# Kernel tuning notes

Measured on AMD Instinct MI355X. Metric: run time of the kernel, lower is better.

Reference implementation:

```python
import jax, jax.numpy as jnp
from jax import lax
import numpy as np

S, B, I, H, O = 65536, 1, 2, 128, 1


def setup_inputs() -> dict:
    key = jax.random.key(0)
    k1, k2, k3, k4 = jax.random.split(key, 4)
    # xavier_normal-style scales
    s_ih = (2.0 / (4 * H + I)) ** 0.5
    s_hh = (2.0 / (4 * H + H)) ** 0.5
    s_out = (2.0 / (H + O)) ** 0.5
    return {
        "x": jax.random.normal(k1, (S, B, I), jnp.float32),
        "h0": jnp.zeros((1, B, H), jnp.float32),
        "c0": jnp.zeros((1, B, H), jnp.float32),
        "W_ih": jax.random.normal(k2, (4 * H, I), jnp.float32) * s_ih,
        "W_hh": jax.random.normal(k3, (4 * H, H), jnp.float32) * s_hh,
        "b_ih": jnp.zeros((4 * H,), jnp.float32),
        "b_hh": jnp.zeros((4 * H,), jnp.float32),
        "W_out": jax.random.normal(k4, (O, H), jnp.float32) * s_out,
        "b_out": jnp.zeros((O,), jnp.float32),
    }


def reference(x, h0, c0, W_ih, W_hh, b_ih, b_hh, W_out, b_out):
    # Precompute input-to-gate projections for all timesteps: (S, B, 4H)
    xg = jnp.einsum("sbi,gi->sbg", x, W_ih) + b_ih + b_hh

    def step(carry, xg_t):
        h, c = carry  # (B, H) each
        gates = xg_t + h @ W_hh.T  # (B, 4H); PyTorch order i,f,g,o
        i, f, g, o = jnp.split(gates, 4, axis=-1)
        i = jax.nn.sigmoid(i)
        f = jax.nn.sigmoid(f)
        g = jnp.tanh(g)
        o = jax.nn.sigmoid(o)
        c = f * c + i * g
        h = o * jnp.tanh(c)
        return (h, c), h

    (_, _), hs = lax.scan(step, (h0[0], c0[0]), xg)  # hs: (S, B, H)
    out = jnp.tanh(hs.transpose(1, 0, 2))  # (B, S, H), matches permute(1,0,2)
    out = out @ W_out.T + b_out  # (B, S, O)
    return out.reshape(out.shape[0] * out.shape[1], -1)  # (B*S, O)
```

## Files before the change

kernel.cpp:

```cpp
#include <hip/hip_runtime.h>

#define S_LEN 65536
#define HDIM 128

typedef _Float16 half2_t __attribute__((ext_vector_type(2)));
typedef _Float16 half8_t __attribute__((ext_vector_type(8)));
typedef float f32x4 __attribute__((ext_vector_type(4)));

__device__ __forceinline__ float sigm(float x) {
    return 1.0f / (1.0f + __expf(-x));
}
__device__ __forceinline__ float tanh_fast(float x) {
    return 2.0f / (1.0f + __expf(-2.0f * x)) - 1.0f;
}
__device__ __forceinline__ float dot2(half2_t a, half2_t b, float c) {
#if __has_builtin(__builtin_amdgcn_fdot2)
    return __builtin_amdgcn_fdot2(a, b, c, false);
#else
    return fmaf((float)a.x, (float)b.x, fmaf((float)a.y, (float)b.y, c));
#endif
}

#define WG_BARRIER() do {                                         \
    asm volatile("s_waitcnt lgkmcnt(0)" ::: "memory");            \
    __builtin_amdgcn_s_barrier();                                 \
    asm volatile("" ::: "memory");                                \
} while (0)

__global__ __launch_bounds__(320)
__attribute__((amdgpu_waves_per_eu(2)))
void lstm_seq_dot2(const float* __restrict__ x,
                   const float* __restrict__ h0,
                   const float* __restrict__ c0,
                   const float* __restrict__ W_ih,
                   const float* __restrict__ W_hh,
                   const float* __restrict__ b_ih,
                   const float* __restrict__ b_hh,
                   _Float16* __restrict__ h_hist)
{
    __shared__ __align__(16) _Float16 h_buf[2][HDIM];
    __shared__ __align__(16) float xb[1024];

    const int tid  = threadIdx.x;
    const int lane = tid & 63;
    const int w    = tid >> 6;

    if (w < 4) {
        const int j    = lane & 31;
        const int half = lane >> 5;
        const int hidx = w * 32 + j;
        const int k0   = half * 64;

#define LW2(g, k2) \
        half2_t w_##g##_##k2; { \
            const float* s_ = W_hh + (size_t)(hidx + 128 * (g)) * HDIM \
                                   + k0 + 2 * (k2); \
            w_##g##_##k2 = (half2_t){ (_Float16)s_[0], (_Float16)s_[1] }; \
            asm volatile("" : "+v"(w_##g##_##k2)); }
#define LWG(g) \
        LW2(g,0)  LW2(g,1)  LW2(g,2)  LW2(g,3)  LW2(g,4)  LW2(g,5)  LW2(g,6)  LW2(g,7)  \
        LW2(g,8)  LW2(g,9)  LW2(g,10) LW2(g,11) LW2(g,12) LW2(g,13) LW2(g,14) LW2(g,15) \
        LW2(g,16) LW2(g,17) LW2(g,18) LW2(g,19) LW2(g,20) LW2(g,21) LW2(g,22) LW2(g,23) \
        LW2(g,24) LW2(g,25) LW2(g,26) LW2(g,27) LW2(g,28) LW2(g,29) LW2(g,30) LW2(g,31)
        LWG(0) LWG(1) LWG(2) LWG(3)
#undef LWG
#undef LW2

        const int r0 = hidx, r1 = hidx + 128, r2 = hidx + 256, r3 = hidx + 384;
        const float wi00 = W_ih[2 * r0], wi01 = W_ih[2 * r0 + 1];
        const float wi10 = W_ih[2 * r1], wi11 = W_ih[2 * r1 + 1];
        const float wi20 = W_ih[2 * r2], wi21 = W_ih[2 * r2 + 1];
        const float wi30 = W_ih[2 * r3], wi31 = W_ih[2 * r3 + 1];
        const float bs0 = b_ih[r0] + b_hh[r0];
        const float bs1 = b_ih[r1] + b_hh[r1];
        const float bs2 = b_ih[r2] + b_hh[r2];
        const float bs3 = b_ih[r3] + b_hh[r3];
        float c = c0[hidx];

        if (tid < HDIM) h_buf[0][tid] = (_Float16)h0[tid];
        __syncthreads();

        const half8_t* hb0 = ((const half8_t*)h_buf[0]) + 8 * half;
        const half8_t* hb1 = ((const half8_t*)h_buf[1]) + 8 * half;

#define PR(hv, p) ((half2_t)__builtin_shufflevector((hv), (hv), 2*(p), 2*(p)+1))

#define GDOT(g, dst) { \
        float A_=0.f, B_=0.f, C_=0.f, D_=0.f; \
        A_=dot2(w_##g##_0 , PR(hv0,0), A_); B_=dot2(w_##g##_1 , PR(hv0,1), B_); \
        C_=dot2(w_##g##_2 , PR(hv0,2), C_); D_=dot2(w_##g##_3 , PR(hv0,3), D_); \
        A_=dot2(w_##g##_4 , PR(hv1,0), A_); B_=dot2(w_##g##_5 , PR(hv1,1), B_); \
        C_=dot2(w_##g##_6 , PR(hv1,2), C_); D_=dot2(w_##g##_7 , PR(hv1,3), D_); \
        A_=dot2(w_##g##_8 , PR(hv2,0), A_); B_=dot2(w_##g##_9 , PR(hv2,1), B_); \
        C_=dot2(w_##g##_10, PR(hv2,2), C_); D_=dot2(w_##g##_11, PR(hv2,3), D_); \
        A_=dot2(w_##g##_12, PR(hv3,0), A_); B_=dot2(w_##g##_13, PR(hv3,1), B_); \
        C_=dot2(w_##g##_14, PR(hv3,2), C_); D_=dot2(w_##g##_15, PR(hv3,3), D_); \
        A_=dot2(w_##g##_16, PR(hv4,0), A_); B_=dot2(w_##g##_17, PR(hv4,1), B_); \
        C_=dot2(w_##g##_18, PR(hv4,2), C_); D_=dot2(w_##g##_19, PR(hv4,3), D_); \
        A_=dot2(w_##g##_20, PR(hv5,0), A_); B_=dot2(w_##g##_21, PR(hv5,1), B_); \
        C_=dot2(w_##g##_22, PR(hv5,2), C_); D_=dot2(w_##g##_23, PR(hv5,3), D_); \
        A_=dot2(w_##g##_24, PR(hv6,0), A_); B_=dot2(w_##g##_25, PR(hv6,1), B_); \
        C_=dot2(w_##g##_26, PR(hv6,2), C_); D_=dot2(w_##g##_27, PR(hv6,3), D_); \
        A_=dot2(w_##g##_28, PR(hv7,0), A_); B_=dot2(w_##g##_29, PR(hv7,1), B_); \
        C_=dot2(w_##g##_30, PR(hv7,2), C_); D_=dot2(w_##g##_31, PR(hv7,3), D_); \
        dst = (A_ + B_) + (C_ + D_); }

#define STEP(T, RB, WB) { \
        const half8_t* hb_ = (RB); \
        half8_t hv0 = hb_[0], hv1 = hb_[1], hv2 = hb_[2], hv3 = hb_[3]; \
        half8_t hv4 = hb_[4], hv5 = hb_[5], hv6 = hb_[6], hv7 = hb_[7]; \
        const float2 xv = *(const float2*)(xb + 2 * ((T) & 511)); \
        float s0, s1, s2, s3; \
        GDOT(1, s1)  s1 += __shfl_xor(s1, 32, 64); \
        GDOT(0, s0)  s0 += __shfl_xor(s0, 32, 64); \
        GDOT(2, s2)  s2 += __shfl_xor(s2, 32, 64); \
        GDOT(3, s3)  s3 += __shfl_xor(s3, 32, 64); \
        const float gf = sigm(fmaf(wi10, xv.x, fmaf(wi11, xv.y, bs1)) + s1); \
        const float gi = sigm(fmaf(wi00, xv.x, fmaf(wi01, xv.y, bs0)) + s0); \
        const float gg = tanh_fast(fmaf(wi20, xv.x, fmaf(wi21, xv.y, bs2)) + s2); \
        const float go = sigm(fmaf(wi30, xv.x, fmaf(wi31, xv.y, bs3)) + s3); \
        c = fmaf(gf, c, gi * gg); \
        const float hval = go * tanh_fast(c); \
        const _Float16 hf_ = (_Float16)hval; \
        if (lane < 32) (WB)[hidx] = hf_; \
        WG_BARRIER(); }

        #pragma unroll 1
        for (int t = 0; t < S_LEN; t += 2) {
            STEP(t,     hb0, h_buf[1])
            STEP(t + 1, hb1, h_buf[0])
        }
#undef STEP
#undef GDOT
#undef PR
    } else {
        {
            const float4* src = (const float4*)x + lane;
            float4 a0 = src[0], a1 = src[64], a2 = src[128], a3 = src[192];
            float4* dst = (float4*)xb + lane;
            dst[0] = a0; dst[64] = a1; dst[128] = a2; dst[192] = a3;
        }
        __syncthreads();

        float4 xs0 = {0.f, 0.f, 0.f, 0.f}, xs1 = xs0;

        #pragma unroll 1
        for (int t = 0; t < S_LEN; ++t) {
            const int r   = t & 255;
            const int blk = t >> 8;
            if (r == 0 && blk >= 1 && blk < 255) {
                const float4* src = (const float4*)x
                                  + (size_t)(blk + 1) * 128 + lane;
                xs0 = src[0]; xs1 = src[64];
            }
            if (r == 128 && blk >= 1 && blk < 255) {
                float4* dst = (float4*)xb + (((blk + 1) & 1) * 128) + lane;
                dst[0] = xs0; dst[64] = xs1;
            }
            if (t > 0) {
                const uint32_t hv_ =
                    *(const uint32_t*)((const char*)(h_buf[t & 1]) + 4 * lane);
                ((uint32_t*)h_hist)[(size_t)(t - 1) * 64 + lane] = hv_;
            }
            WG_BARRIER();
        }
        const uint32_t hv_ =
            *(const uint32_t*)((const char*)(h_buf[0]) + 4 * lane);
        ((uint32_t*)h_hist)[(size_t)(S_LEN - 1) * 64 + lane] = hv_;
    }
}

__global__ __launch_bounds__(256)
void out_proj(const _Float16* __restrict__ h_hist,
              const float* __restrict__ W_out,
              const float* __restrict__ b_out,
              float* __restrict__ out)
{
    const int lane  = threadIdx.x & 63;
    const int gwave = (blockIdx.x * 256 + threadIdx.x) >> 6;
    const int nwave = (gridDim.x * 256) >> 6;

    const float wo0 = W_out[2 * lane + 0];
    const float wo1 = W_out[2 * lane + 1];
    const float bout = b_out[0];

    for (int t = gwave; t < S_LEN; t += nwave) {
        half2_t hv = ((const half2_t*)(h_hist + t * HDIM))[lane];
        float p = tanh_fast((float)hv.x) * wo0 + tanh_fast((float)hv.y) * wo1;
        #pragma unroll
        for (int off = 32; off > 0; off >>= 1)
            p += __shfl_xor(p, off, 64);
        if (lane == 0) out[t] = p + bout;
    }
}

#define H_HI_OFF 144
__global__ __launch_bounds__(1024)
__attribute__((amdgpu_waves_per_eu(4, 4)))
void lstm_seq_full(const float* __restrict__ x,
                   const float* __restrict__ h0,
                   const float* __restrict__ c0,
                   const float* __restrict__ W_ih,
                   const float* __restrict__ W_hh,
                   const float* __restrict__ b_ih,
                   const float* __restrict__ b_hh,
                   const float* __restrict__ W_out,
                   const float* __restrict__ b_out,
                   float* __restrict__ out)
{
    __shared__ __align__(16) unsigned char h_raw[2 * H_HI_OFF];
    __shared__ float gates_part[2 * 512];
    __shared__ float red_sh[2];

    const int tid  = threadIdx.x;
    const int j    = tid >> 1;
    const int half = tid & 1;

    const float2* wr2 = (const float2*)(W_hh + j * HDIM + half * 64);
#define WDEF(i) half2_t W##i; { float2 t = wr2[i]; \
        W##i.x = (_Float16)t.x; W##i.y = (_Float16)t.y; } \
        asm volatile("" : "+v"(W##i));
    WDEF(0)  WDEF(1)  WDEF(2)  WDEF(3)  WDEF(4)  WDEF(5)  WDEF(6)  WDEF(7)
    WDEF(8)  WDEF(9)  WDEF(10) WDEF(11) WDEF(12) WDEF(13) WDEF(14) WDEF(15)
    WDEF(16) WDEF(17) WDEF(18) WDEF(19) WDEF(20) WDEF(21) WDEF(22) WDEF(23)
    WDEF(24) WDEF(25) WDEF(26) WDEF(27) WDEF(28) WDEF(29) WDEF(30) WDEF(31)
#undef WDEF

    float wih0 = 0.0f, wih1 = 0.0f, bias = 0.0f;
    if (half == 0) {
        wih0 = W_ih[2 * j + 0];
        wih1 = W_ih[2 * j + 1];
        bias = b_ih[j] + b_hh[j];
    }

    float c = 0.0f, wout = 0.0f;
    _Float16* hw = (_Float16*)(h_raw + ((tid < 64) ? 2 * tid
                                                   : H_HI_OFF + 2 * (tid - 64)));
    if (tid < HDIM) {
        c = c0[tid];
        wout = W_out[tid];
        *hw = (_Float16)h0[tid];
    }
    const float bout = b_out[0];
    __syncthreads();

    const float2* xp = (const float2*)x;
    float2 xcur = xp[0];
    const half8_t* hp = (const half8_t*)(h_raw + half * H_HI_OFF);

    #pragma unroll 1
    for (int t = 0; t < S_LEN; ++t) {
        const int tn = (t + 1 < S_LEN) ? (t + 1) : (S_LEN - 1);
        float2 xnext = xp[tn];

        float a0 = fmaf(wih0, xcur.x, fmaf(wih1, xcur.y, bias));
        float a1 = 0.0f, a2 = 0.0f, a3 = 0.0f;

#define CHUNK(cc, w0_, w1_, w2_, w3_) {                         \
        half8_t hv = hp[cc];                                    \
        half2_t p0 = { hv[0], hv[1] };                          \
        half2_t p1 = { hv[2], hv[3] };                          \
        half2_t p2 = { hv[4], hv[5] };                          \
        half2_t p3 = { hv[6], hv[7] };                          \
        a0 = dot2(w0_, p0, a0);                                 \
        a1 = dot2(w1_, p1, a1);                                 \
        a2 = dot2(w2_, p2, a2);                                 \
        a3 = dot2(w3_, p3, a3); }
        CHUNK(0, W0,  W1,  W2,  W3)
        CHUNK(1, W4,  W5,  W6,  W7)
        CHUNK(2, W8,  W9,  W10, W11)
        CHUNK(3, W12, W13, W14, W15)
        CHUNK(4, W16, W17, W18, W19)
        CHUNK(5, W20, W21, W22, W23)
        CHUNK(6, W24, W25, W26, W27)
        CHUNK(7, W28, W29, W30, W31)
#undef CHUNK

        gates_part[half * 512 + j] = (a0 + a1) + (a2 + a3);
        __syncthreads();

        if (tid < HDIM) {
            float gi = sigm(gates_part[tid]            + gates_part[tid + 512]);
            float gf = sigm(gates_part[tid + 128]      + gates_part[tid + 640]);
            float gg = tanh_fast(gates_part[tid + 256] + gates_part[tid + 768]);
            float go = sigm(gates_part[tid + 384]      + gates_part[tid + 896]);
            c = fmaf(gf, c, gi * gg);
            float h = go * tanh_fast(c);
            *hw = (_Float16)h;

            float p = tanh_fast(h) * wout;
            #pragma unroll
            for (int off = 32; off > 0; off >>= 1)
                p += __shfl_xor(p, off, 64);
            if ((tid & 63) == 0) red_sh[tid >> 6] = p;
        }
        __syncthreads();

        if (tid == 0) out[t] = red_sh[0] + red_sh[1] + bout;
        xcur = xnext;
    }
}

extern "C" void kernel_launch(void* const* d_in, const int* in_sizes, int n_in,
                              void* d_out, int out_size, void* d_ws, size_t ws_size,
                              hipStream_t stream) {
    const float* x     = (const float*)d_in[0];
    const float* h0    = (const float*)d_in[1];
    const float* c0    = (const float*)d_in[2];
    const float* W_ih  = (const float*)d_in[3];
    const float* W_hh  = (const float*)d_in[4];
    const float* b_ih  = (const float*)d_in[5];
    const float* b_hh  = (const float*)d_in[6];
    const float* W_out = (const float*)d_in[7];
    const float* b_out = (const float*)d_in[8];

    const size_t need = (size_t)S_LEN * HDIM * sizeof(_Float16);
    if (ws_size >= need) {
        _Float16* h_hist = (_Float16*)d_ws;
        lstm_seq_dot2<<<dim3(1), dim3(320), 0, stream>>>(
            x, h0, c0, W_ih, W_hh, b_ih, b_hh, h_hist);
        out_proj<<<dim3(1024), dim3(256), 0, stream>>>(
            h_hist, W_out, b_out, (float*)d_out);
    } else {
        lstm_seq_full<<<dim3(1), dim3(1024), 0, stream>>>(
            x, h0, c0, W_ih, W_hh, b_ih, b_hh, W_out, b_out, (float*)d_out);
    }
}
```

Before: 42.00 ms.

## Split LSTM recurrence dot products across four K-quarters with eight compute waves

Reworks the single-workgroup recurrent kernel so eight compute waves (instead of four) each handle 16 hidden units, with each unit's 128-long dot product split into four 32-element quarters across lane groups, reduced by two xor shuffles. This halves the serial dot2 chain per lane per step, shortening the latency of each of the 65536 sequential timesteps. The cost is more waves synchronising at every barrier and an extra shuffle stage per gate. The helper wave that stages x inputs is now wave 8.

```diff
diff --git a/kernel.cpp b/kernel.cpp
--- a/kernel.cpp
+++ b/kernel.cpp
@@ -5,7 +5,6 @@
 
 typedef _Float16 half2_t __attribute__((ext_vector_type(2)));
 typedef _Float16 half8_t __attribute__((ext_vector_type(8)));
-typedef float f32x4 __attribute__((ext_vector_type(4)));
 
 __device__ __forceinline__ float sigm(float x) {
     return 1.0f / (1.0f + __expf(-x));
@@ -21,22 +20,26 @@
 #endif
 }
 
+__device__ __forceinline__ float xor32_add(float v) {
+    return v + __shfl_xor(v, 32, 64);
+}
+
 #define WG_BARRIER() do {                                         \
     asm volatile("s_waitcnt lgkmcnt(0)" ::: "memory");            \
     __builtin_amdgcn_s_barrier();                                 \
     asm volatile("" ::: "memory");                                \
 } while (0)
 
-__global__ __launch_bounds__(320)
-__attribute__((amdgpu_waves_per_eu(2)))
-void lstm_seq_dot2(const float* __restrict__ x,
-                   const float* __restrict__ h0,
-                   const float* __restrict__ c0,
-                   const float* __restrict__ W_ih,
-                   const float* __restrict__ W_hh,
-                   const float* __restrict__ b_ih,
-                   const float* __restrict__ b_hh,
-                   _Float16* __restrict__ h_hist)
+__global__ __launch_bounds__(576)
+__attribute__((amdgpu_waves_per_eu(3)))
+void lstm_seq_q(const float* __restrict__ x,
+                const float* __restrict__ h0,
+                const float* __restrict__ c0,
+                const float* __restrict__ W_ih,
+                const float* __restrict__ W_hh,
+                const float* __restrict__ b_ih,
+                const float* __restrict__ b_hh,
+                _Float16* __restrict__ h_hist)
 {
     __shared__ __align__(16) _Float16 h_buf[2][HDIM];
     __shared__ __align__(16) float xb[1024];
@@ -45,28 +48,27 @@
     const int lane = tid & 63;
     const int w    = tid >> 6;
 
-    if (w < 4) {
-        const int j    = lane & 31;
-        const int half = lane >> 5;
-        const int hidx = w * 32 + j;
-        const int k0   = half * 64;
-
-#define LW2(g, k2) \
-        half2_t w_##g##_##k2; { \
-            const float* s_ = W_hh + (size_t)(hidx + 128 * (g)) * HDIM \
-                                   + k0 + 2 * (k2); \
-            w_##g##_##k2 = (half2_t){ (_Float16)s_[0], (_Float16)s_[1] }; \
-            asm volatile("" : "+v"(w_##g##_##k2)); }
+    if (w < 8) {
+        const int j = lane & 15;
+        const int q = lane >> 4;
+        const int e = 16 * w + j;
+
+#define LW2(g, k) \
+        half2_t w_##g##_##k; { \
+            const float* s_ = W_hh + (size_t)(e + 128 * (g)) * HDIM \
+                                   + 32 * q + 2 * (k); \
+            w_##g##_##k = (half2_t){ (_Float16)s_[0], (_Float16)s_[1] }; \
+            asm volatile("" : "+v"(w_##g##_##k)); }
 #define LWG(g) \
-        LW2(g,0)  LW2(g,1)  LW2(g,2)  LW2(g,3)  LW2(g,4)  LW2(g,5)  LW2(g,6)  LW2(g,7)  \
-        LW2(g,8)  LW2(g,9)  LW2(g,10) LW2(g,11) LW2(g,12) LW2(g,13) LW2(g,14) LW2(g,15) \
-        LW2(g,16) LW2(g,17) LW2(g,18) LW2(g,19) LW2(g,20) LW2(g,21) LW2(g,22) LW2(g,23) \
-        LW2(g,24) LW2(g,25) LW2(g,26) LW2(g,27) LW2(g,28) LW2(g,29) LW2(g,30) LW2(g,31)
+        LW2(g,0)  LW2(g,1)  LW2(g,2)  LW2(g,3)  \
+        LW2(g,4)  LW2(g,5)  LW2(g,6)  LW2(g,7)  \
+        LW2(g,8)  LW2(g,9)  LW2(g,10) LW2(g,11) \
+        LW2(g,12) LW2(g,13) LW2(g,14) LW2(g,15)
         LWG(0) LWG(1) LWG(2) LWG(3)
 #undef LWG
 #undef LW2
 
-        const int r0 = hidx, r1 = hidx + 128, r2 = hidx + 256, r3 = hidx + 384;
+        const int r0 = e, r1 = e + 128, r2 = e + 256, r3 = e + 384;
         const float wi00 = W_ih[2 * r0], wi01 = W_ih[2 * r0 + 1];
         const float wi10 = W_ih[2 * r1], wi11 = W_ih[2 * r1 + 1];
         const float wi20 = W_ih[2 * r2], wi21 = W_ih[2 * r2 + 1];
@@ -75,60 +77,51 @@
         const float bs1 = b_ih[r1] + b_hh[r1];
         const float bs2 = b_ih[r2] + b_hh[r2];
         const float bs3 = b_ih[r3] + b_hh[r3];
-        float c = c0[hidx];
+        float c = c0[e];
 
         if (tid < HDIM) h_buf[0][tid] = (_Float16)h0[tid];
         __syncthreads();
 
-        const half8_t* hb0 = ((const half8_t*)h_buf[0]) + 8 * half;
-        const half8_t* hb1 = ((const half8_t*)h_buf[1]) + 8 * half;
-
 #define PR(hv, p) ((half2_t)__builtin_shufflevector((hv), (hv), 2*(p), 2*(p)+1))
 
 #define GDOT(g, dst) { \
-        float A_=0.f, B_=0.f, C_=0.f, D_=0.f; \
-        A_=dot2(w_##g##_0 , PR(hv0,0), A_); B_=dot2(w_##g##_1 , PR(hv0,1), B_); \
-        C_=dot2(w_##g##_2 , PR(hv0,2), C_); D_=dot2(w_##g##_3 , PR(hv0,3), D_); \
-        A_=dot2(w_##g##_4 , PR(hv1,0), A_); B_=dot2(w_##g##_5 , PR(hv1,1), B_); \
-        C_=dot2(w_##g##_6 , PR(hv1,2), C_); D_=dot2(w_##g##_7 , PR(hv1,3), D_); \
-        A_=dot2(w_##g##_8 , PR(hv2,0), A_); B_=dot2(w_##g##_9 , PR(hv2,1), B_); \
-        C_=dot2(w_##g##_10, PR(hv2,2), C_); D_=dot2(w_##g##_11, PR(hv2,3), D_); \
-        A_=dot2(w_##g##_12, PR(hv3,0), A_); B_=dot2(w_##g##_13, PR(hv3,1), B_); \
-        C_=dot2(w_##g##_14, PR(hv3,2), C_); D_=dot2(w_##g##_15, PR(hv3,3), D_); \
-        A_=dot2(w_##g##_16, PR(hv4,0), A_); B_=dot2(w_##g##_17, PR(hv4,1), B_); \
-        C_=dot2(w_##g##_18, PR(hv4,2), C_); D_=dot2(w_##g##_19, PR(hv4,3), D_); \
-        A_=dot2(w_##g##_20, PR(hv5,0), A_); B_=dot2(w_##g##_21, PR(hv5,1), B_); \
-        C_=dot2(w_##g##_22, PR(hv5,2), C_); D_=dot2(w_##g##_23, PR(hv5,3), D_); \
-        A_=dot2(w_##g##_24, PR(hv6,0), A_); B_=dot2(w_##g##_25, PR(hv6,1), B_); \
-        C_=dot2(w_##g##_26, PR(hv6,2), C_); D_=dot2(w_##g##_27, PR(hv6,3), D_); \
-        A_=dot2(w_##g##_28, PR(hv7,0), A_); B_=dot2(w_##g##_29, PR(hv7,1), B_); \
-        C_=dot2(w_##g##_30, PR(hv7,2), C_); D_=dot2(w_##g##_31, PR(hv7,3), D_); \
-        dst = (A_ + B_) + (C_ + D_); }
+        float A_ = 0.f, B_ = 0.f; \
+        A_=dot2(w_##g##_0 , PR(hc0,0), A_); B_=dot2(w_##g##_1 , PR(hc0,1), B_); \
+        A_=dot2(w_##g##_2 , PR(hc0,2), A_); B_=dot2(w_##g##_3 , PR(hc0,3), B_); \
+        A_=dot2(w_##g##_4 , PR(hc1,0), A_); B_=dot2(w_##g##_5 , PR(hc1,1), B_); \
+        A_=dot2(w_##g##_6 , PR(hc1,2), A_); B_=dot2(w_##g##_7 , PR(hc1,3), B_); \
+        A_=dot2(w_##g##_8 , PR(hc2,0), A_); B_=dot2(w_##g##_9 , PR(hc2,1), B_); \
+        A_=dot2(w_##g##_10, PR(hc2,2), A_); B_=dot2(w_##g##_11, PR(hc2,3), B_); \
+        A_=dot2(w_##g##_12, PR(hc3,0), A_); B_=dot2(w_##g##_13, PR(hc3,1), B_); \
+        A_=dot2(w_##g##_14, PR(hc3,2), A_); B_=dot2(w_##g##_15, PR(hc3,3), B_); \
+        dst = A_ + B_; }
 
 #define STEP(T, RB, WB) { \
-        const half8_t* hb_ = (RB); \
-        half8_t hv0 = hb_[0], hv1 = hb_[1], hv2 = hb_[2], hv3 = hb_[3]; \
-        half8_t hv4 = hb_[4], hv5 = hb_[5], hv6 = hb_[6], hv7 = hb_[7]; \
+        const half8_t* hb_ = (const half8_t*)(RB) + 4 * q; \
+        half8_t hc0 = hb_[0], hc1 = hb_[1], hc2 = hb_[2], hc3 = hb_[3]; \
         const float2 xv = *(const float2*)(xb + 2 * ((T) & 511)); \
         float s0, s1, s2, s3; \
-        GDOT(1, s1)  s1 += __shfl_xor(s1, 32, 64); \
-        GDOT(0, s0)  s0 += __shfl_xor(s0, 32, 64); \
-        GDOT(2, s2)  s2 += __shfl_xor(s2, 32, 64); \
-        GDOT(3, s3)  s3 += __shfl_xor(s3, 32, 64); \
+        GDOT(1, s1)  s1 += __shfl_xor(s1, 16, 64); \
+        GDOT(0, s0)  s0 += __shfl_xor(s0, 16, 64); \
+        GDOT(2, s2)  s2 += __shfl_xor(s2, 16, 64); \
+        GDOT(3, s3)  s3 += __shfl_xor(s3, 16, 64); \
+        s1 = xor32_add(s1); \
+        s0 = xor32_add(s0); \
+        s2 = xor32_add(s2); \
+        s3 = xor32_add(s3); \
         const float gf = sigm(fmaf(wi10, xv.x, fmaf(wi11, xv.y, bs1)) + s1); \
         const float gi = sigm(fmaf(wi00, xv.x, fmaf(wi01, xv.y, bs0)) + s0); \
         const float gg = tanh_fast(fmaf(wi20, xv.x, fmaf(wi21, xv.y, bs2)) + s2); \
         const float go = sigm(fmaf(wi30, xv.x, fmaf(wi31, xv.y, bs3)) + s3); \
         c = fmaf(gf, c, gi * gg); \
         const float hval = go * tanh_fast(c); \
-        const _Float16 hf_ = (_Float16)hval; \
-        if (lane < 32) (WB)[hidx] = hf_; \
+        if (q == 0) (WB)[e] = (_Float16)hval; \
         WG_BARRIER(); }
 
         #pragma unroll 1
         for (int t = 0; t < S_LEN; t += 2) {
-            STEP(t,     hb0, h_buf[1])
-            STEP(t + 1, hb1, h_buf[0])
+            STEP(t,     h_buf[0], h_buf[1])
+            STEP(t + 1, h_buf[1], h_buf[0])
         }
 #undef STEP
 #undef GDOT
@@ -317,7 +310,7 @@
     const size_t need = (size_t)S_LEN * HDIM * sizeof(_Float16);
     if (ws_size >= need) {
         _Float16* h_hist = (_Float16*)d_ws;
-        lstm_seq_dot2<<<dim3(1), dim3(320), 0, stream>>>(
+        lstm_seq_q<<<dim3(1), dim3(576), 0, stream>>>(
             x, h0, c0, W_ih, W_hh, b_ih, b_hh, h_hist);
         out_proj<<<dim3(1024), dim3(256), 0, stream>>>(
             h_hist, W_out, b_out, (float*)d_out);
```

New measurement: 53.00 ms. 1.26x slower.
